# Performance work log

Measured on AMD Instinct MI355X. Metric: run time of the kernel, lower is better.

Reference implementation:

```python
import jax, jax.numpy as jnp
import numpy as np

B, N, D, H, C = 32, 128, 32, 64, 10
P = 2 * H + 1  # pair feature dim


def setup_inputs() -> dict:
    key = jax.random.key(0)
    ks = jax.random.split(key, 20)
    f32 = jnp.float32

    def w(k, i, o):
        return (jax.random.normal(k, (i, o), f32) / np.sqrt(i)).astype(f32)

    def bvec(k, o):
        return (jax.random.normal(k, (o,), f32) * 0.02).astype(f32)

    return {
        "x": jax.random.normal(ks[0], (B, N, D), f32),
        "adj": jax.random.uniform(ks[1], (B, N, N), f32),
        # 1-GNN layer 1 (D->H): W1 self, W2 neighbor
        "w11": w(ks[2], D, H), "b11": bvec(ks[3], H),
        "w12": w(ks[4], D, H), "b12": bvec(ks[5], H),
        # 1-GNN layer 2 (H->H)
        "w21": w(ks[6], H, H), "b21": bvec(ks[7], H),
        "w22": w(ks[8], H, H), "b22": bvec(ks[9], H),
        # 2-GNN layer 1 (P->H)
        "p1w1": w(ks[10], P, H), "p1b1": bvec(ks[11], H),
        "p1w2": w(ks[12], P, H), "p1b2": bvec(ks[13], H),
        # 2-GNN layer 2 (H->H)
        "p2w1": w(ks[14], H, H), "p2b1": bvec(ks[15], H),
        "p2w2": w(ks[16], H, H), "p2b2": bvec(ks[17], H),
        # classifier (2H -> C)
        "cw": w(ks[18], 2 * H, C), "cb": bvec(ks[19], C),
    }


def _lin(h, W, b):
    return h @ W + b


def _forward(x, adj, w11, b11, w12, b12, w21, b21, w22, b22,
             p1w1, p1b1, p1w2, p1b2, p2w1, p2b1, p2w2, p2b2, cw, cb):
    n = x.shape[1]
    # ---- dense 1-GNN: h = relu(W1 h + A W2 h) ----
    h = jax.nn.relu(_lin(x, w11, b11) + jnp.einsum('bij,bjd->bid', adj, _lin(x, w12, b12)))
    h = jax.nn.relu(_lin(h, w21, b21) + jnp.einsum('bij,bjd->bid', adj, _lin(h, w22, b22)))
    emb1 = h.sum(axis=1)  # [B,H]

    # ---- dense 2-GNN ----
    eye = jnp.eye(n, dtype=adj.dtype)
    adj_clean = adj * (1.0 - eye)[None]  # zero diagonal
    ii, jj = jnp.meshgrid(jnp.arange(n), jnp.arange(n), indexing='ij')
    imin = jnp.minimum(ii, jj)  # canonical min-index node of pair
    imax = jnp.maximum(ii, jj)
    first = h[:, imin, :]   # [B,N,N,H] = h at min(i,j)
    second = h[:, imax, :]  # [B,N,N,H] = h at max(i,j)
    pair = jnp.concatenate([first, second, adj_clean[..., None]], axis=-1)  # [B,N,N,P]

    for (W1, b1, W2, b2) in ((p1w1, p1b1, p1w2, p1b2), (p2w1, p2b1, p2w2, p2b2)):
        g = _lin(pair, W2, b2)          # [B,N,N,H]
        self_part = _lin(pair, W1, b1)  # [B,N,N,H]
        agg1 = jnp.einsum('biw,bjwd->bijd', adj_clean, g)
        agg2 = jnp.einsum('bjw,biwd->bijd', adj_clean, g)
        pair = jax.nn.relu(self_part + agg1 + agg2)

    upper = jnp.triu(jnp.ones((n, n), dtype=pair.dtype), k=1)
    emb2 = (pair * upper[None, :, :, None]).sum(axis=(1, 2))  # [B,H]

    return jnp.concatenate([emb1, emb2], axis=1) @ cw + cb  # [B,C]


def reference(x, adj, w11, b11, w12, b12, w21, b21, w22, b22,
              p1w1, p1b1, p1w2, p1b2, p2w1, p2b1, p2w2, p2b2, cw, cb):
    return _forward(x, adj, w11, b11, w12, b12, w21, b21, w22, b22,
                    p1w1, p1b1, p1w2, p1b2, p2w1, p2b1, p2w2, p2b2, cw, cb)
```

## Files before the change

kernel.cpp:

```cpp
#include <hip/hip_runtime.h>

#define B 32
#define N 128
#define DD 32
#define H 64
#define C 10

typedef unsigned short bfu;
typedef __attribute__((ext_vector_type(8))) short bf16x8;
typedef __attribute__((ext_vector_type(4))) float f32x4;

#define MFMA16 __builtin_amdgcn_mfma_f32_16x16x32_bf16

__device__ __forceinline__ float b2f(bfu v) {
    union { unsigned u; float f; } x; x.u = ((unsigned)v) << 16; return x.f;
}
__device__ __forceinline__ bfu f2b(float f) {
    union { __bf16 b; bfu u; } c; c.b = (__bf16)f; return c.u;
}
__device__ __forceinline__ float lo2f(unsigned u) {
    union { unsigned x; float f; } c; c.x = u << 16; return c.f;
}
__device__ __forceinline__ float hi2f(unsigned u) {
    union { unsigned x; float f; } c; c.x = u & 0xffff0000u; return c.f;
}
__device__ __forceinline__ void up8(uint4 u, float* f) {
    f[0] = lo2f(u.x); f[1] = hi2f(u.x); f[2] = lo2f(u.y); f[3] = hi2f(u.y);
    f[4] = lo2f(u.z); f[5] = hi2f(u.z); f[6] = lo2f(u.w); f[7] = hi2f(u.w);
}
__device__ __forceinline__ unsigned pk2(float a, float b) {
    return (unsigned)f2b(a) | ((unsigned)f2b(b) << 16);
}

__global__ __launch_bounds__(256) void prep_acadj(const float* __restrict__ adj,
                                                  bfu* __restrict__ acb,
                                                  bfu* __restrict__ adjf) {
    int idx = blockIdx.x * 256 + threadIdx.x;
    float4 v = ((const float4*)adj)[idx];
    int e0 = idx * 4;
    int w = e0 & 127;
    int i = (e0 >> 7) & 127;
    ushort4 o;
    o.x = f2b((i == w    ) ? 0.f : v.x);
    o.y = f2b((i == w + 1) ? 0.f : v.y);
    o.z = f2b((i == w + 2) ? 0.f : v.z);
    o.w = f2b((i == w + 3) ? 0.f : v.w);
    ((ushort4*)acb)[idx] = o;
    ushort4 oF;
    oF.x = f2b(v.x); oF.y = f2b(v.y); oF.z = f2b(v.z); oF.w = f2b(v.w);
    ((ushort4*)adjf)[idx] = oF;
}

struct WT { const float* src[10]; bfu* dst[10]; int K[10]; };
__global__ __launch_bounds__(256) void prep_wtN(WT p) {
    int m = blockIdx.x;
    const float* S = p.src[m];
    bfu* D = p.dst[m];
    int K = p.K[m];
    int t = threadIdx.x; int d = t & 63;
    for (int k = t >> 6; k < K; k += 4)
        D[d * K + k] = f2b(S[k * 64 + d]);
}

__global__ __launch_bounds__(256) void gnn_front(const float* __restrict__ x,
                                                 const bfu* __restrict__ adjf,
                                                 const bfu* __restrict__ w11t,
                                                 const float* __restrict__ b11,
                                                 const bfu* __restrict__ w12t,
                                                 const float* __restrict__ b12,
                                                 const bfu* __restrict__ w21t,
                                                 const float* __restrict__ b21,
                                                 const bfu* __restrict__ w22t,
                                                 const float* __restrict__ b22,
                                                 const bfu* __restrict__ u1t,
                                                 const bfu* __restrict__ v1t,
                                                 const bfu* __restrict__ u2t,
                                                 const bfu* __restrict__ v2t,
                                                 bfu* __restrict__ U1,
                                                 bfu* __restrict__ V1,
                                                 bfu* __restrict__ U2,
                                                 bfu* __restrict__ V2,
                                                 float* __restrict__ emb1) {
    int b = blockIdx.x;
    int t = threadIdx.x, lane = t & 63, wid = t >> 6;
    int l16 = lane & 15, g4 = lane >> 4;
    __shared__ bfu Af[128 * 136];
    __shared__ bfu Yt[64 * 136];
    __shared__ bfu Hs[128 * 72];
    __shared__ bfu Xs[128 * 40];
    __shared__ float red[16][64];
    {
        int i = t >> 1, half = t & 1;
        const uint4* src = (const uint4*)(adjf + ((size_t)b * N + i) * N + half * 64);
        uint4* dst = (uint4*)&Af[i * 136 + half * 64];
#pragma unroll
        for (int q = 0; q < 8; ++q) dst[q] = src[q];
        const float4* sx = (const float4*)(x + ((size_t)b * N + i) * DD + half * 16);
        float xv[16];
        *(float4*)&xv[0]  = sx[0]; *(float4*)&xv[4]  = sx[1];
        *(float4*)&xv[8]  = sx[2]; *(float4*)&xv[12] = sx[3];
        unsigned q[8];
#pragma unroll
        for (int e = 0; e < 8; ++e) q[e] = pk2(xv[2 * e], xv[2 * e + 1]);
        uint4* dx = (uint4*)&Xs[i * 40 + half * 16];
        dx[0] = make_uint4(q[0], q[1], q[2], q[3]);
        dx[1] = make_uint4(q[4], q[5], q[6], q[7]);
    }
    __syncthreads();
    f32x4 a1[2][4], a2[2][4];
#define ZERO(A) _Pragma("unroll") for (int m = 0; m < 2; ++m) _Pragma("unroll") for (int n = 0; n < 4; ++n) A[m][n] = (f32x4){0.f,0.f,0.f,0.f};
    ZERO(a1); ZERO(a2);
    {
        int k0 = g4 * 8;
        bf16x8 bw1[4], bw2[4];
#pragma unroll
        for (int n = 0; n < 4; ++n) {
            bw1[n] = *(const bf16x8*)&w11t[(l16 + 16 * n) * 32 + k0];
            bw2[n] = *(const bf16x8*)&w12t[(l16 + 16 * n) * 32 + k0];
        }
#pragma unroll
        for (int m = 0; m < 2; ++m) {
            bf16x8 afr = *(const bf16x8*)&Xs[(wid * 32 + m * 16 + l16) * 40 + k0];
#pragma unroll
            for (int n = 0; n < 4; ++n) {
                a1[m][n] = MFMA16(afr, bw1[n], a1[m][n], 0, 0, 0);
                a2[m][n] = MFMA16(afr, bw2[n], a2[m][n], 0, 0, 0);
            }
        }
    }
    {
        float bb[4];
#pragma unroll
        for (int n = 0; n < 4; ++n) bb[n] = b12[l16 + 16 * n];
#pragma unroll
        for (int m = 0; m < 2; ++m)
#pragma unroll
            for (int n = 0; n < 4; ++n) {
                uint2 q;
                q.x = pk2(a2[m][n][0] + bb[n], a2[m][n][1] + bb[n]);
                q.y = pk2(a2[m][n][2] + bb[n], a2[m][n][3] + bb[n]);
                *(uint2*)&Yt[(l16 + 16 * n) * 136 + wid * 32 + m * 16 + g4 * 4] = q;
            }
    }
    __syncthreads();
    ZERO(a2);
#pragma unroll
    for (int ks = 0; ks < 4; ++ks) {
        int k0 = ks * 32 + g4 * 8;
        bf16x8 bfr[4];
#pragma unroll
        for (int n = 0; n < 4; ++n) bfr[n] = *(const bf16x8*)&Yt[(l16 + 16 * n) * 136 + k0];
#pragma unroll
        for (int m = 0; m < 2; ++m) {
            bf16x8 afr = *(const bf16x8*)&Af[(wid * 32 + m * 16 + l16) * 136 + k0];
#pragma unroll
            for (int n = 0; n < 4; ++n) a2[m][n] = MFMA16(afr, bfr[n], a2[m][n], 0, 0, 0);
        }
    }
    {
        float bb[4];
#pragma unroll
        for (int n = 0; n < 4; ++n) bb[n] = b11[l16 + 16 * n];
#pragma unroll
        for (int m = 0; m < 2; ++m)
#pragma unroll
            for (int n = 0; n < 4; ++n)
#pragma unroll
                for (int r = 0; r < 4; ++r)
                    Hs[(wid * 32 + m * 16 + g4 * 4 + r) * 72 + l16 + 16 * n] =
                        f2b(fmaxf(a1[m][n][r] + bb[n] + a2[m][n][r], 0.f));
    }
    __syncthreads();
    ZERO(a1); ZERO(a2);
#pragma unroll
    for (int ks = 0; ks < 2; ++ks) {
        int k0 = ks * 32 + g4 * 8;
        bf16x8 bw1[4], bw2[4];
#pragma unroll
        for (int n = 0; n < 4; ++n) {
            bw1[n] = *(const bf16x8*)&w21t[(l16 + 16 * n) * 64 + k0];
            bw2[n] = *(const bf16x8*)&w22t[(l16 + 16 * n) * 64 + k0];
        }
#pragma unroll
        for (int m = 0; m < 2; ++m) {
            bf16x8 afr = *(const bf16x8*)&Hs[(wid * 32 + m * 16 + l16) * 72 + k0];
#pragma unroll
            for (int n = 0; n < 4; ++n) {
                a1[m][n] = MFMA16(afr, bw1[n], a1[m][n], 0, 0, 0);
                a2[m][n] = MFMA16(afr, bw2[n], a2[m][n], 0, 0, 0);
            }
        }
    }
    {
        float bb[4];
#pragma unroll
        for (int n = 0; n < 4; ++n) bb[n] = b22[l16 + 16 * n];
#pragma unroll
        for (int m = 0; m < 2; ++m)
#pragma unroll
            for (int n = 0; n < 4; ++n) {
                uint2 q;
                q.x = pk2(a2[m][n][0] + bb[n], a2[m][n][1] + bb[n]);
                q.y = pk2(a2[m][n][2] + bb[n], a2[m][n][3] + bb[n]);
                *(uint2*)&Yt[(l16 + 16 * n) * 136 + wid * 32 + m * 16 + g4 * 4] = q;
            }
    }
    __syncthreads();
    ZERO(a2);
#pragma unroll
    for (int ks = 0; ks < 4; ++ks) {
        int k0 = ks * 32 + g4 * 8;
        bf16x8 bfr[4];
#pragma unroll
        for (int n = 0; n < 4; ++n) bfr[n] = *(const bf16x8*)&Yt[(l16 + 16 * n) * 136 + k0];
#pragma unroll
        for (int m = 0; m < 2; ++m) {
            bf16x8 afr = *(const bf16x8*)&Af[(wid * 32 + m * 16 + l16) * 136 + k0];
#pragma unroll
            for (int n = 0; n < 4; ++n) a2[m][n] = MFMA16(afr, bfr[n], a2[m][n], 0, 0, 0);
        }
    }
    {
        float bb[4], s[4] = {0.f, 0.f, 0.f, 0.f};
#pragma unroll
        for (int n = 0; n < 4; ++n) bb[n] = b21[l16 + 16 * n];
#pragma unroll
        for (int m = 0; m < 2; ++m)
#pragma unroll
            for (int n = 0; n < 4; ++n)
#pragma unroll
                for (int r = 0; r < 4; ++r) {
                    float v = fmaxf(a1[m][n][r] + bb[n] + a2[m][n][r], 0.f);
                    Hs[(wid * 32 + m * 16 + g4 * 4 + r) * 72 + l16 + 16 * n] = f2b(v);
                    s[n] += v;
                }
#pragma unroll
        for (int n = 0; n < 4; ++n) red[wid * 4 + g4][l16 + 16 * n] = s[n];
    }
    __syncthreads();
    if (t < 64) {
        float e = 0.f;
#pragma unroll
        for (int q = 0; q < 16; ++q) e += red[q][t];
        emb1[b * 64 + t] = e;
    }
    const bfu* wts[4] = {u1t, v1t, u2t, v2t};
    bfu* outs[4] = {U1, V1, U2, V2};
#pragma unroll
    for (int o = 0; o < 4; ++o) {
        ZERO(a1);
#pragma unroll
        for (int ks = 0; ks < 2; ++ks) {
            int k0 = ks * 32 + g4 * 8;
            bf16x8 bw[4];
#pragma unroll
            for (int n = 0; n < 4; ++n)
                bw[n] = *(const bf16x8*)&wts[o][(l16 + 16 * n) * 64 + k0];
#pragma unroll
            for (int m = 0; m < 2; ++m) {
                bf16x8 afr = *(const bf16x8*)&Hs[(wid * 32 + m * 16 + l16) * 72 + k0];
#pragma unroll
                for (int n = 0; n < 4; ++n) a1[m][n] = MFMA16(afr, bw[n], a1[m][n], 0, 0, 0);
            }
        }
#pragma unroll
        for (int m = 0; m < 2; ++m)
#pragma unroll
            for (int n = 0; n < 4; ++n)
#pragma unroll
                for (int r = 0; r < 4; ++r)
                    Af[(wid * 32 + m * 16 + g4 * 4 + r) * 72 + l16 + 16 * n] = f2b(a1[m][n][r]);
        __syncthreads();
        {
            int i = t >> 1, half = t & 1;
            const uint4* src = (const uint4*)&Af[i * 72 + half * 32];
            uint4* dst = (uint4*)(outs[o] + ((size_t)b * N + i) * H + half * 32);
            dst[0] = src[0]; dst[1] = src[1]; dst[2] = src[2]; dst[3] = src[3];
        }
        __syncthreads();
    }
#undef ZERO
}

__global__ __launch_bounds__(64) void rowsum_kernel(const float* __restrict__ in,
                                                    float* __restrict__ out) {
    int b = blockIdx.x;
    int d = threadIdx.x;
    float acc = 0.f;
#pragma unroll 8
    for (int n = 0; n < N; ++n) acc += in[((size_t)b * N + n) * H + d];
    out[(size_t)b * H + d] = acc;
}

__global__ __launch_bounds__(256) void t1_mfma(const bfu* __restrict__ U2,
                                               const bfu* __restrict__ V2,
                                               const bfu* __restrict__ acb,
                                               const float* __restrict__ wl,
                                               const float* __restrict__ bv,
                                               bfu* __restrict__ T, int b0) {
    int bl = blockIdx.x >> 7, j = blockIdx.x & 127;
    int b = b0 + bl;
    int t = threadIdx.x, lane = t & 63, wid = t >> 6;
    int l16 = lane & 15, g4 = lane >> 4;
    __shared__ bfu lds[128 * 72];
    __shared__ float arl[N];
    const bfu* arow = acb + ((size_t)b * N + j) * N;
    if (t < N) arl[t] = b2f(arow[t]);
    __syncthreads();
    {
        int d = lane;
        const bfu* U2b = U2 + (size_t)b * N * H;
        const bfu* V2b = V2 + (size_t)b * N * H;
        float wld = wl[d], bvd = bv[d];
        float UjB = b2f(U2b[j * H + d]) + bvd, VjB = b2f(V2b[j * H + d]) + bvd;
#pragma unroll
        for (int p = 0; p < 4; ++p) {
            int w0 = p * 32 + wid * 8;
            unsigned q[4];
#pragma unroll
            for (int rr = 0; rr < 4; ++rr) {
                float g01[2];
#pragma unroll
                for (int hh = 0; hh < 2; ++hh) {
                    int w = w0 + rr * 2 + hh;
                    float a = arl[w];
                    float rvar = (w < j) ? b2f(U2b[w * H + d]) : b2f(V2b[w * H + d]);
                    float base = (w < j) ? VjB : UjB;
                    g01[hh] = rvar + base + a * wld;
                }
                q[rr] = pk2(g01[0], g01[1]);
            }
            *(uint4*)&lds[d * 136 + w0] = make_uint4(q[0], q[1], q[2], q[3]);
        }
    }
    __syncthreads();
    f32x4 acc[2][4];
#pragma unroll
    for (int m = 0; m < 2; ++m)
#pragma unroll
        for (int n = 0; n < 4; ++n) acc[m][n] = (f32x4){0.f, 0.f, 0.f, 0.f};
    const bfu* Ab = acb + (size_t)b * N * N;
#pragma unroll
    for (int ks = 0; ks < 4; ++ks) {
        int k0 = ks * 32 + g4 * 8;
        bf16x8 bfr[4];
#pragma unroll
        for (int n = 0; n < 4; ++n)
            bfr[n] = *(const bf16x8*)&lds[(l16 + 16 * n) * 136 + k0];
#pragma unroll
        for (int m = 0; m < 2; ++m) {
            int i = wid * 32 + m * 16 + l16;
            bf16x8 afr = *(const bf16x8*)&Ab[(size_t)i * N + k0];
#pragma unroll
            for (int n = 0; n < 4; ++n)
                acc[m][n] = MFMA16(afr, bfr[n], acc[m][n], 0, 0, 0);
        }
    }
    __syncthreads();
#pragma unroll
    for (int m = 0; m < 2; ++m)
#pragma unroll
        for (int n = 0; n < 4; ++n)
#pragma unroll
            for (int r = 0; r < 4; ++r)
                lds[(wid * 32 + m * 16 + g4 * 4 + r) * 72 + l16 + 16 * n] = f2b(acc[m][n][r]);
    __syncthreads();
    {
        int i = t >> 1, half = t & 1;
        const uint4* src = (const uint4*)&lds[i * 72 + half * 32];
        uint4* dst = (uint4*)(T + (((size_t)bl * N + j) * N + i) * H + half * 32);
        dst[0] = src[0]; dst[1] = src[1]; dst[2] = src[2]; dst[3] = src[3];
    }
}

__device__ __forceinline__ void build_P2(bfu* Pl, const bfu* U1b,
                                         const bfu* V1b, const bfu* arow,
                                         const bfu* Trow, const bfu* Tcol,
                                         const float* wl1, const float* bv1,
                                         int c, int t) {
    int wq = t >> 3, d0 = (t & 7) * 8;
    float wv[8], bvv[8], UcB[8], VcB[8];
    *(float4*)&wv[0]  = *(const float4*)(wl1 + d0);
    *(float4*)&wv[4]  = *(const float4*)(wl1 + d0 + 4);
    *(float4*)&bvv[0] = *(const float4*)(bv1 + d0);
    *(float4*)&bvv[4] = *(const float4*)(bv1 + d0 + 4);
    up8(*(const uint4*)&U1b[c * H + d0], UcB);
    up8(*(const uint4*)&V1b[c * H + d0], VcB);
#pragma unroll
    for (int e = 0; e < 8; ++e) { UcB[e] += bvv[e]; VcB[e] += bvv[e]; }
#pragma unroll
    for (int p = 0; p < 4; ++p) {
        int w = p * 32 + wq;
        float a = b2f(arow[w]);
        const bfu* rs = (w < c) ? U1b : V1b;
        float rv[8], tc[8], tw[8];
        up8(*(const uint4*)&rs[w * H + d0], rv);
        up8(*(const uint4*)&Trow[(size_t)w * H + d0], tc);
        up8(*(const uint4*)&Tcol[(size_t)w * N * H + d0], tw);
        unsigned q[4];
#pragma unroll
        for (int e = 0; e < 4; ++e) {
            float b0 = (w < c) ? VcB[2 * e] : UcB[2 * e];
            float b1 = (w < c) ? VcB[2 * e + 1] : UcB[2 * e + 1];
            float p0 = fmaxf(rv[2 * e]     + b0 + a * wv[2 * e]     + tc[2 * e]     + tw[2 * e],     0.f);
            float p1 = fmaxf(rv[2 * e + 1] + b1 + a * wv[2 * e + 1] + tc[2 * e + 1] + tw[2 * e + 1], 0.f);
            q[e] = pk2(p0, p1);
        }
        *(uint4*)&Pl[w * 72 + d0] = make_uint4(q[0], q[1], q[2], q[3]);
    }
}

__global__ __launch_bounds__(256) void t2_fused(const bfu* __restrict__ U1,
                                                const bfu* __restrict__ V1,
                                                const bfu* __restrict__ acb,
                                                const float* __restrict__ wl1,
                                                const float* __restrict__ bv1,
                                                const bfu* __restrict__ T1,
                                                const bfu* __restrict__ W2t,
                                                const float* __restrict__ bv2,
                                                bfu* __restrict__ T2, int b0) {
    int bl = blockIdx.x >> 7, j = blockIdx.x & 127;
    int b = b0 + bl;
    int t = threadIdx.x, lane = t & 63, wid = t >> 6;
    int l16 = lane & 15, g4 = lane >> 4;
    __shared__ bfu P[128 * 72];
    __shared__ bfu Gt[64 * 136];
    const bfu* T1b = T1 + (size_t)bl * N * N * H;
    build_P2(P, U1 + (size_t)b * N * H, V1 + (size_t)b * N * H,
             acb + ((size_t)b * N + j) * N,
             T1b + (size_t)j * N * H, T1b + (size_t)j * H,
             wl1, bv1, j, t);
    __syncthreads();
    f32x4 acc[2][4];
#pragma unroll
    for (int m = 0; m < 2; ++m)
#pragma unroll
        for (int n = 0; n < 4; ++n) acc[m][n] = (f32x4){0.f, 0.f, 0.f, 0.f};
#pragma unroll
    for (int ks = 0; ks < 2; ++ks) {
        int k0 = ks * 32 + g4 * 8;
        bf16x8 bw[4];
#pragma unroll
        for (int n = 0; n < 4; ++n)
            bw[n] = *(const bf16x8*)&W2t[(l16 + 16 * n) * 64 + k0];
#pragma unroll
        for (int m = 0; m < 2; ++m) {
            bf16x8 afr = *(const bf16x8*)&P[(wid * 32 + m * 16 + l16) * 72 + k0];
#pragma unroll
            for (int n = 0; n < 4; ++n)
                acc[m][n] = MFMA16(afr, bw[n], acc[m][n], 0, 0, 0);
        }
    }
    {
        float bb[4];
#pragma unroll
        for (int n = 0; n < 4; ++n) bb[n] = bv2[l16 + 16 * n];
#pragma unroll
        for (int m = 0; m < 2; ++m)
#pragma unroll
            for (int n = 0; n < 4; ++n) {
                uint2 q;
                q.x = pk2(acc[m][n][0] + bb[n], acc[m][n][1] + bb[n]);
                q.y = pk2(acc[m][n][2] + bb[n], acc[m][n][3] + bb[n]);
                *(uint2*)&Gt[(l16 + 16 * n) * 136 + wid * 32 + m * 16 + g4 * 4] = q;
            }
    }
    __syncthreads();
#pragma unroll
    for (int m = 0; m < 2; ++m)
#pragma unroll
        for (int n = 0; n < 4; ++n) acc[m][n] = (f32x4){0.f, 0.f, 0.f, 0.f};
    const bfu* Ab = acb + (size_t)b * N * N;
#pragma unroll
    for (int ks = 0; ks < 4; ++ks) {
        int k0 = ks * 32 + g4 * 8;
        bf16x8 bfr[4];
#pragma unroll
        for (int n = 0; n < 4; ++n)
            bfr[n] = *(const bf16x8*)&Gt[(l16 + 16 * n) * 136 + k0];
#pragma unroll
        for (int m = 0; m < 2; ++m) {
            int i = wid * 32 + m * 16 + l16;
            bf16x8 afr = *(const bf16x8*)&Ab[(size_t)i * N + k0];
#pragma unroll
            for (int n = 0; n < 4; ++n)
                acc[m][n] = MFMA16(afr, bfr[n], acc[m][n], 0, 0, 0);
        }
    }
#pragma unroll
    for (int m = 0; m < 2; ++m)
#pragma unroll
        for (int n = 0; n < 4; ++n)
#pragma unroll
            for (int r = 0; r < 4; ++r)
                P[(wid * 32 + m * 16 + g4 * 4 + r) * 72 + l16 + 16 * n] = f2b(acc[m][n][r]);
    __syncthreads();
    {
        int i = t >> 1, half = t & 1;
        const uint4* src = (const uint4*)&P[i * 72 + half * 32];
        uint4* dst = (uint4*)(T2 + (((size_t)bl * N + j) * N + i) * H + half * 32);
        dst[0] = src[0]; dst[1] = src[1]; dst[2] = src[2]; dst[3] = src[3];
    }
}

__global__ __launch_bounds__(256) void combine2_fused(const bfu* __restrict__ U1,
                                                      const bfu* __restrict__ V1,
                                                      const bfu* __restrict__ acb,
                                                      const float* __restrict__ wl1,
                                                      const float* __restrict__ bv1,
                                                      const bfu* __restrict__ T1,
                                                      const bfu* __restrict__ W1t,
                                                      const float* __restrict__ bv2,
                                                      const bfu* __restrict__ T2,
                                                      float* __restrict__ part2, int b0) {
    int bl = blockIdx.x >> 7, i = blockIdx.x & 127;
    int b = b0 + bl;
    int t = threadIdx.x, lane = t & 63, wid = t >> 6;
    int l16 = lane & 15, g4 = lane >> 4;
    __shared__ bfu P[128 * 72];
    __shared__ float red[32][64];
    const bfu* T1b = T1 + (size_t)bl * N * N * H;
    build_P2(P, U1 + (size_t)b * N * H, V1 + (size_t)b * N * H,
             acb + ((size_t)b * N + i) * N,
             T1b + (size_t)i * N * H, T1b + (size_t)i * H,
             wl1, bv1, i, t);
    __syncthreads();
    f32x4 acc[2][4];
#pragma unroll
    for (int m = 0; m < 2; ++m)
#pragma unroll
        for (int n = 0; n < 4; ++n) acc[m][n] = (f32x4){0.f, 0.f, 0.f, 0.f};
#pragma unroll
    for (int ks = 0; ks < 2; ++ks) {
        int k0 = ks * 32 + g4 * 8;
        bf16x8 bw[4];
#pragma unroll
        for (int n = 0; n < 4; ++n)
            bw[n] = *(const bf16x8*)&W1t[(l16 + 16 * n) * 64 + k0];
#pragma unroll
        for (int m = 0; m < 2; ++m) {
            bf16x8 afr = *(const bf16x8*)&P[(wid * 32 + m * 16 + l16) * 72 + k0];
#pragma unroll
            for (int n = 0; n < 4; ++n)
                acc[m][n] = MFMA16(afr, bw[n], acc[m][n], 0, 0, 0);
        }
    }
    {
        float bb[4];
#pragma unroll
        for (int n = 0; n < 4; ++n) bb[n] = bv2[l16 + 16 * n];
#pragma unroll
        for (int m = 0; m < 2; ++m)
#pragma unroll
            for (int n = 0; n < 4; ++n)
#pragma unroll
                for (int r = 0; r < 4; ++r)
                    P[(wid * 32 + m * 16 + g4 * 4 + r) * 72 + l16 + 16 * n] =
                        f2b(acc[m][n][r] + bb[n]);
    }
    __syncthreads();
    int dc = t & 7, jg = t >> 3, d0 = dc * 8;
    float ps[8];
#pragma unroll
    for (int e = 0; e < 8; ++e) ps[e] = 0.f;
    const bfu* T2b = T2 + (size_t)bl * N * N * H;
#pragma unroll
    for (int r = 0; r < 4; ++r) {
        int j = jg + r * 32;
        if (j > i) {
            float ti[8], tj[8], sv[8];
            up8(*(const uint4*)&T2b[((size_t)i * N + j) * H + d0], ti);
            up8(*(const uint4*)&T2b[((size_t)j * N + i) * H + d0], tj);
            up8(*(const uint4*)&P[j * 72 + d0], sv);
#pragma unroll
            for (int e = 0; e < 8; ++e)
                ps[e] += fmaxf(sv[e] + ti[e] + tj[e], 0.f);
        }
    }
#pragma unroll
    for (int e = 0; e < 8; ++e) red[jg][d0 + e] = ps[e];
    __syncthreads();
    if (t < 64) {
        float s = 0.f;
#pragma unroll 8
        for (int g = 0; g < 32; ++g) s += red[g][t];
        part2[((size_t)b * N + i) * H + t] = s;
    }
}

__global__ __launch_bounds__(64) void final_kernel(const float* __restrict__ emb1,
                                                   const float* __restrict__ emb2,
                                                   const float* __restrict__ cw,
                                                   const float* __restrict__ cb,
                                                   float* __restrict__ out) {
    int b = blockIdx.x;
    int c = threadIdx.x;
    if (c < C) {
        float acc = cb[c];
#pragma unroll 8
        for (int k = 0; k < H; ++k) acc += emb1[(size_t)b * H + k] * cw[(size_t)k * C + c];
#pragma unroll 8
        for (int k = 0; k < H; ++k) acc += emb2[(size_t)b * H + k] * cw[(size_t)(H + k) * C + c];
        out[(size_t)b * C + c] = acc;
    }
}

extern "C" void kernel_launch(void* const* d_in, const int* in_sizes, int n_in,
                              void* d_out, int out_size, void* d_ws, size_t ws_size,
                              hipStream_t stream) {
    const float* x    = (const float*)d_in[0];
    const float* adj  = (const float*)d_in[1];
    const float* w11  = (const float*)d_in[2];
    const float* b11  = (const float*)d_in[3];
    const float* w12  = (const float*)d_in[4];
    const float* b12  = (const float*)d_in[5];
    const float* w21  = (const float*)d_in[6];
    const float* b21  = (const float*)d_in[7];
    const float* w22  = (const float*)d_in[8];
    const float* b22  = (const float*)d_in[9];
    const float* p1w1 = (const float*)d_in[10];
    const float* p1b1 = (const float*)d_in[11];
    const float* p1w2 = (const float*)d_in[12];
    const float* p1b2 = (const float*)d_in[13];
    const float* p2w1 = (const float*)d_in[14];
    const float* p2b1 = (const float*)d_in[15];
    const float* p2w2 = (const float*)d_in[16];
    const float* p2b2 = (const float*)d_in[17];
    const float* cw   = (const float*)d_in[18];
    const float* cb   = (const float*)d_in[19];
    float* out = (float*)d_out;

    const size_t NBH = (size_t)B * N * H;
    const size_t BIG = (size_t)N * N * H;

    float* part2 = (float*)d_ws;
    float* emb1  = part2 + NBH;
    float* emb2  = emb1 + (size_t)B * H;
    bfu* U1   = (bfu*)(emb2 + (size_t)B * H);
    bfu* V1   = U1 + NBH;
    bfu* U2   = V1 + NBH;
    bfu* V2   = U2 + NBH;
    bfu* acb  = V2 + NBH;
    bfu* adjf = acb + (size_t)B * N * N;
    bfu* w11t = adjf + (size_t)B * N * N;
    bfu* w12t = w11t + 32 * 64;
    bfu* w21t = w12t + 32 * 64;
    bfu* w22t = w21t + 64 * 64;
    bfu* u1t  = w22t + 64 * 64;
    bfu* v1t  = u1t + 64 * 64;
    bfu* u2t  = v1t + 64 * 64;
    bfu* v2t  = u2t + 64 * 64;
    bfu* W1t  = v2t + 64 * 64;
    bfu* W2t  = W1t + 64 * 64;
    bfu* bigBase = W2t + 64 * 64;
    size_t smallBytes = (char*)bigBase - (char*)d_ws;

    int CB = B;
    while (CB > 1 && smallBytes + 2ull * CB * BIG * sizeof(bfu) > ws_size) CB >>= 1;
    bfu* T1 = bigBase;
    bfu* T2 = T1 + (size_t)CB * BIG;

    prep_acadj<<<dim3(B * N * N / 1024), 256, 0, stream>>>(adj, acb, adjf);
    {
        WT p;
        const float* srcs[10] = {w11, w12, w21, w22,
                                 p1w1, p1w1 + 64 * H, p1w2, p1w2 + 64 * H,
                                 p2w1, p2w2};
        bfu* dsts[10] = {w11t, w12t, w21t, w22t, u1t, v1t, u2t, v2t, W1t, W2t};
        int Ks[10] = {32, 32, 64, 64, 64, 64, 64, 64, 64, 64};
        for (int q = 0; q < 10; ++q) { p.src[q] = srcs[q]; p.dst[q] = dsts[q]; p.K[q] = Ks[q]; }
        prep_wtN<<<dim3(10), 256, 0, stream>>>(p);
    }
    gnn_front<<<dim3(B), 256, 0, stream>>>(x, adjf, w11t, b11, w12t, b12,
                                           w21t, b21, w22t, b22,
                                           u1t, v1t, u2t, v2t,
                                           U1, V1, U2, V2, emb1);
    for (int b0 = 0; b0 < B; b0 += CB) {
        dim3 cg(CB * N);
        t1_mfma<<<cg, 256, 0, stream>>>(U2, V2, acb, p1w2 + 128 * H, p1b2, T1, b0);
        t2_fused<<<cg, 256, 0, stream>>>(U1, V1, acb, p1w1 + 128 * H, p1b1,
                                         T1, W2t, p2b2, T2, b0);
        combine2_fused<<<cg, 256, 0, stream>>>(U1, V1, acb, p1w1 + 128 * H, p1b1,
                                               T1, W1t, p2b1, T2, part2, b0);
    }

    rowsum_kernel<<<B, 64, 0, stream>>>(part2, emb2);
    final_kernel<<<B, 64, 0, stream>>>(emb1, emb2, cw, cb, out);
}
```

Measured before the change: 177.8 us.

## Merge prep and tail kernels, add XCD-aware block swizzle to pair kernels

Fuses the adjacency conversion and weight transpose into one prep launch, and merges the rowsum and classifier kernels into a single tail kernel, cutting two launches. It also remaps block indices in the three pair-stage kernels so that consecutive logical blocks (same batch) land on the same XCD, aiming for better L2 reuse of per-batch data. The swizzle assumes the grid size is divisible by 8, which holds for the CB*128 grids used here.

```diff
diff --git a/kernel.cpp b/kernel.cpp
--- a/kernel.cpp
+++ b/kernel.cpp
@@ -32,34 +32,35 @@
     return (unsigned)f2b(a) | ((unsigned)f2b(b) << 16);
 }
 
-__global__ __launch_bounds__(256) void prep_acadj(const float* __restrict__ adj,
-                                                  bfu* __restrict__ acb,
-                                                  bfu* __restrict__ adjf) {
-    int idx = blockIdx.x * 256 + threadIdx.x;
-    float4 v = ((const float4*)adj)[idx];
-    int e0 = idx * 4;
-    int w = e0 & 127;
-    int i = (e0 >> 7) & 127;
-    ushort4 o;
-    o.x = f2b((i == w    ) ? 0.f : v.x);
-    o.y = f2b((i == w + 1) ? 0.f : v.y);
-    o.z = f2b((i == w + 2) ? 0.f : v.z);
-    o.w = f2b((i == w + 3) ? 0.f : v.w);
-    ((ushort4*)acb)[idx] = o;
-    ushort4 oF;
-    oF.x = f2b(v.x); oF.y = f2b(v.y); oF.z = f2b(v.z); oF.w = f2b(v.w);
-    ((ushort4*)adjf)[idx] = oF;
-}
-
 struct WT { const float* src[10]; bfu* dst[10]; int K[10]; };
-__global__ __launch_bounds__(256) void prep_wtN(WT p) {
-    int m = blockIdx.x;
-    const float* S = p.src[m];
-    bfu* D = p.dst[m];
-    int K = p.K[m];
-    int t = threadIdx.x; int d = t & 63;
-    for (int k = t >> 6; k < K; k += 4)
-        D[d * K + k] = f2b(S[k * 64 + d]);
+__global__ __launch_bounds__(256) void prep_all(const float* __restrict__ adj,
+                                                bfu* __restrict__ acb,
+                                                bfu* __restrict__ adjf, WT p) {
+    int blk = blockIdx.x;
+    if (blk < 512) {
+        int idx = blk * 256 + threadIdx.x;
+        float4 v = ((const float4*)adj)[idx];
+        int e0 = idx * 4;
+        int w = e0 & 127;
+        int i = (e0 >> 7) & 127;
+        ushort4 o;
+        o.x = f2b((i == w    ) ? 0.f : v.x);
+        o.y = f2b((i == w + 1) ? 0.f : v.y);
+        o.z = f2b((i == w + 2) ? 0.f : v.z);
+        o.w = f2b((i == w + 3) ? 0.f : v.w);
+        ((ushort4*)acb)[idx] = o;
+        ushort4 oF;
+        oF.x = f2b(v.x); oF.y = f2b(v.y); oF.z = f2b(v.z); oF.w = f2b(v.w);
+        ((ushort4*)adjf)[idx] = oF;
+    } else {
+        int m = blk - 512;
+        const float* S = p.src[m];
+        bfu* D = p.dst[m];
+        int K = p.K[m];
+        int t = threadIdx.x; int d = t & 63;
+        for (int k = t >> 6; k < K; k += 4)
+            D[d * K + k] = f2b(S[k * 64 + d]);
+    }
 }
 
 __global__ __launch_bounds__(256) void gnn_front(const float* __restrict__ x,
@@ -282,14 +283,8 @@
 #undef ZERO
 }
 
-__global__ __launch_bounds__(64) void rowsum_kernel(const float* __restrict__ in,
-                                                    float* __restrict__ out) {
-    int b = blockIdx.x;
-    int d = threadIdx.x;
-    float acc = 0.f;
-#pragma unroll 8
-    for (int n = 0; n < N; ++n) acc += in[((size_t)b * N + n) * H + d];
-    out[(size_t)b * H + d] = acc;
+__device__ __forceinline__ int xcd_swz(int wg, int nwg) {
+    return (wg & 7) * (nwg >> 3) + (wg >> 3);
 }
 
 __global__ __launch_bounds__(256) void t1_mfma(const bfu* __restrict__ U2,
@@ -298,7 +293,8 @@
                                                const float* __restrict__ wl,
                                                const float* __restrict__ bv,
                                                bfu* __restrict__ T, int b0) {
-    int bl = blockIdx.x >> 7, j = blockIdx.x & 127;
+    int wid2 = xcd_swz(blockIdx.x, gridDim.x);
+    int bl = wid2 >> 7, j = wid2 & 127;
     int b = b0 + bl;
     int t = threadIdx.x, lane = t & 63, wid = t >> 6;
     int l16 = lane & 15, g4 = lane >> 4;
@@ -419,7 +415,8 @@
                                                 const bfu* __restrict__ W2t,
                                                 const float* __restrict__ bv2,
                                                 bfu* __restrict__ T2, int b0) {
-    int bl = blockIdx.x >> 7, j = blockIdx.x & 127;
+    int wid2 = xcd_swz(blockIdx.x, gridDim.x);
+    int bl = wid2 >> 7, j = wid2 & 127;
     int b = b0 + bl;
     int t = threadIdx.x, lane = t & 63, wid = t >> 6;
     int l16 = lane & 15, g4 = lane >> 4;
@@ -513,7 +510,8 @@
                                                       const float* __restrict__ bv2,
                                                       const bfu* __restrict__ T2,
                                                       float* __restrict__ part2, int b0) {
-    int bl = blockIdx.x >> 7, i = blockIdx.x & 127;
+    int wid2 = xcd_swz(blockIdx.x, gridDim.x);
+    int bl = wid2 >> 7, i = wid2 & 127;
     int b = b0 + bl;
     int t = threadIdx.x, lane = t & 63, wid = t >> 6;
     int l16 = lane & 15, g4 = lane >> 4;
@@ -588,20 +586,27 @@
     }
 }
 
-__global__ __launch_bounds__(64) void final_kernel(const float* __restrict__ emb1,
-                                                   const float* __restrict__ emb2,
-                                                   const float* __restrict__ cw,
-                                                   const float* __restrict__ cb,
-                                                   float* __restrict__ out) {
+__global__ __launch_bounds__(64) void tail_kernel(const float* __restrict__ part2,
+                                                  const float* __restrict__ emb1,
+                                                  const float* __restrict__ cw,
+                                                  const float* __restrict__ cb,
+                                                  float* __restrict__ out) {
     int b = blockIdx.x;
-    int c = threadIdx.x;
-    if (c < C) {
-        float acc = cb[c];
+    int d = threadIdx.x;
+    __shared__ float e2[64];
+    float acc = 0.f;
 #pragma unroll 8
-        for (int k = 0; k < H; ++k) acc += emb1[(size_t)b * H + k] * cw[(size_t)k * C + c];
+    for (int n = 0; n < N; ++n) acc += part2[((size_t)b * N + n) * H + d];
+    e2[d] = acc;
+    __syncthreads();
+    if (d < C) {
+        float o = cb[d];
 #pragma unroll 8
-        for (int k = 0; k < H; ++k) acc += emb2[(size_t)b * H + k] * cw[(size_t)(H + k) * C + c];
-        out[(size_t)b * C + c] = acc;
+        for (int k = 0; k < H; ++k) {
+            o += emb1[(size_t)b * H + k] * cw[(size_t)k * C + d];
+            o += e2[k] * cw[(size_t)(H + k) * C + d];
+        }
+        out[(size_t)b * C + d] = o;
     }
 }
 
@@ -660,7 +665,6 @@
     bfu* T1 = bigBase;
     bfu* T2 = T1 + (size_t)CB * BIG;
 
-    prep_acadj<<<dim3(B * N * N / 1024), 256, 0, stream>>>(adj, acb, adjf);
     {
         WT p;
         const float* srcs[10] = {w11, w12, w21, w22,
@@ -669,7 +673,7 @@
         bfu* dsts[10] = {w11t, w12t, w21t, w22t, u1t, v1t, u2t, v2t, W1t, W2t};
         int Ks[10] = {32, 32, 64, 64, 64, 64, 64, 64, 64, 64};
         for (int q = 0; q < 10; ++q) { p.src[q] = srcs[q]; p.dst[q] = dsts[q]; p.K[q] = Ks[q]; }
-        prep_wtN<<<dim3(10), 256, 0, stream>>>(p);
+        prep_all<<<dim3(512 + 10), 256, 0, stream>>>(adj, acb, adjf, p);
     }
     gnn_front<<<dim3(B), 256, 0, stream>>>(x, adjf, w11t, b11, w12t, b12,
                                            w21t, b21, w22t, b22,
@@ -683,7 +687,5 @@
         combine2_fused<<<cg, 256, 0, stream>>>(U1, V1, acb, p1w1 + 128 * H, p1b1,
                                                T1, W1t, p2b1, T2, part2, b0);
     }
-
-    rowsum_kernel<<<B, 64, 0, stream>>>(part2, emb2);
-    final_kernel<<<B, 64, 0, stream>>>(emb1, emb2, cw, cb, out);
-}
+    tail_kernel<<<dim3(B), 64, 0, stream>>>(part2, emb1, cw, cb, out);
+}
```

After: 165.7 us. 6.8% less time.
